# Optimization experiments

Measured on AMD Instinct MI355X. Metric: run time of the kernel, lower is better.

Reference implementation:

```python
import jax, jax.numpy as jnp
import numpy as np

B, S, D, H, HD = 2, 2048, 768, 12, 64


def setup_inputs() -> dict:
    key = jax.random.key(0)
    ks = jax.random.split(key, 8)
    w = lambda k, shp: jax.random.normal(k, shp, dtype=jnp.float32) * 0.02
    return {
        "hidden_states": jax.random.normal(ks[0], (B, S, D), dtype=jnp.float32),
        "Wq": w(ks[1], (D, D)), "bq": jnp.zeros((D,), jnp.float32),
        "Wk": w(ks[2], (D, D)), "bk": jnp.zeros((D,), jnp.float32),
        "Wv": w(ks[3], (D, D)), "bv": jnp.zeros((D,), jnp.float32),
        # hedgehog feature maps are initialized to identity in the module
        "Wfq": jnp.eye(HD, dtype=jnp.float32) + w(ks[4], (HD, HD)),
        "bfq": jnp.zeros((HD,), jnp.float32),
        "Wfk": jnp.eye(HD, dtype=jnp.float32) + w(ks[5], (HD, HD)),
        "bfk": jnp.zeros((HD,), jnp.float32),
    }


def _heads(x):
    # [B,S,D] -> [B,H,S,HD]
    return x.reshape(B, S, H, HD).transpose(0, 2, 1, 3)


def _feature_map(x, Wf, bf):
    # exp / exp(-x) hedgehog map: [B,H,S,HD] -> [B,H,S,2*HD]
    y = jnp.einsum('bhsd,ed->bhse', x, Wf) + bf
    return jnp.concatenate([jnp.exp(y), jnp.exp(-y)], axis=-1)


def reference(hidden_states, Wq, bq, Wk, bk, Wv, bv, Wfq, bfq, Wfk, bfk):
    h = hidden_states
    q = _heads(h @ Wq.T + bq)   # [B,H,S,HD]
    k = _heads(h @ Wk.T + bk)
    v = _heads(h @ Wv.T + bv)

    # frozen base (softmax) attention producing outputs + true_attns
    scale = 1.0 / np.sqrt(HD).astype(np.float32)
    scores = jnp.einsum('bhmd,bhnd->bhmn', q, k) * scale
    true_attns = jax.nn.softmax(scores, axis=-1)
    out = jnp.einsum('bhmn,bhnd->bhmd', true_attns, v)
    outputs = out.transpose(0, 2, 1, 3).reshape(B, S, D)

    # hedgehog predicted attention: quadratic linear attention
    fq = _feature_map(q, Wfq, bfq)  # [B,H,S,2*HD]
    fk = _feature_map(k, Wfk, bfk)
    qk = jnp.einsum('bhmd,bhnd->bhmn', fq, fk)
    pred_attns = qk / qk.sum(axis=-1, keepdims=True)

    return outputs, pred_attns, true_attns
```

## Files before the change

### kernel.cpp

```cpp
#include <hip/hip_runtime.h>
#include <math.h>

namespace {

constexpr int kB = 2, kS = 2048, kD = 768, kH = 12, kHD = 64, kF = 128, kBH = kB * kH;

typedef __attribute__((ext_vector_type(8))) short short8;
typedef __attribute__((ext_vector_type(4))) short short4v;
typedef __attribute__((ext_vector_type(4))) float f32x4;

__device__ __forceinline__ ushort f2bf(float x) {
    union { float f; unsigned u; } v; v.f = x;
    return (ushort)((v.u + 0x7fffu + ((v.u >> 16) & 1u)) >> 16);
}
__device__ __forceinline__ float bf2f(ushort u) {
    union { unsigned u; float f; } v; v.u = ((unsigned)u) << 16; return v.f;
}

__device__ __forceinline__ void gload16(const ushort* g, void* lds) {
    __builtin_amdgcn_global_load_lds(
        (const __attribute__((address_space(1))) void*)g,
        (__attribute__((address_space(3))) void*)lds, 16, 0, 0);
}

__device__ __forceinline__ void gstage64x64(ushort* ldsBase, const ushort* g,
                                            size_t strideElems, int w, int lane) {
    #pragma unroll
    for (int j = 0; j < 2; ++j) {
        const int row = 16 * w + 8 * j + (lane >> 3);
        const int chunk = lane & 7;
        const ushort* gp = g + (size_t)row * strideElems + ((chunk ^ (row & 7)) * 8);
        void* lp = (char*)ldsBase + (16 * w + 8 * j) * 128;
        gload16(gp, lp);
    }
}

__device__ __forceinline__ void gstageA128(ushort* ldsBase, const ushort* g,
                                           size_t strideElems, int w, int lane) {
    #pragma unroll
    for (int j = 0; j < 4; ++j) {
        const int row = 32 * w + 8 * j + (lane >> 3);
        const int chunk = lane & 7;
        const ushort* gp = g + (size_t)row * strideElems + ((chunk ^ (row & 7)) * 8);
        void* lp = (char*)ldsBase + (32 * w + 8 * j) * 128;
        gload16(gp, lp);
    }
}

__device__ __forceinline__ void gstage64x128(ushort* ldsBase, const ushort* g,
                                             int w, int lane) {
    #pragma unroll
    for (int j = 0; j < 4; ++j) {
        const int row = 16 * w + 4 * j + (lane >> 4);
        const int chunk = lane & 15;
        const ushort* gp = g + (size_t)row * kF + ((chunk ^ (row & 7)) * 8);
        void* lp = (char*)ldsBase + (16 * w + 4 * j) * 256;
        gload16(gp, lp);
    }
}

__device__ __forceinline__ void stage64x64(ushort* dst, const ushort* srcRow0,
                                           size_t rowStride, int t) {
    const int row = t >> 2, ce = (t & 3) * 16;
    const ushort* s = srcRow0 + (size_t)row * rowStride + ce;
    uint4 u0 = *(const uint4*)s;
    uint4 u1 = *(const uint4*)(s + 8);
    const int sw = (row & 7) << 4;
    *(uint4*)((char*)dst + row * 128 + ((ce * 2) ^ sw)) = u0;
    *(uint4*)((char*)dst + row * 128 + ((ce * 2 + 16) ^ sw)) = u1;
}

__device__ __forceinline__ void stage64x128(ushort* dst, const ushort* srcRow0, int t) {
    const int row = t >> 2, ce = (t & 3) * 32;
    const ushort* s = srcRow0 + (size_t)row * kF + ce;
    const int sw = (row & 7) << 4;
    #pragma unroll
    for (int u = 0; u < 4; ++u) {
        uint4 x = *(const uint4*)(s + u * 8);
        *(uint4*)((char*)dst + row * 256 + ((ce * 2 + u * 16) ^ sw)) = x;
    }
}

__global__ __launch_bounds__(256) void cast_kernel(
    const float* __restrict__ s0, const float* __restrict__ s1,
    const float* __restrict__ s2, const float* __restrict__ s3,
    ushort* __restrict__ d0, ushort* __restrict__ d1,
    ushort* __restrict__ d2, ushort* __restrict__ d3)
{
    const int seg = blockIdx.y;
    const float* src = seg == 0 ? s0 : seg == 1 ? s1 : seg == 2 ? s2 : s3;
    ushort* dst      = seg == 0 ? d0 : seg == 1 ? d1 : seg == 2 ? d2 : d3;
    const int n4 = (seg == 0 ? kB * kS * kD : kD * kD) / 4;
    for (int i = blockIdx.x * 256 + threadIdx.x; i < n4; i += gridDim.x * 256) {
        float4 v = *(const float4*)&src[(size_t)i * 4];
        short4v o;
        o[0] = (short)f2bf(v.x); o[1] = (short)f2bf(v.y);
        o[2] = (short)f2bf(v.z); o[3] = (short)f2bf(v.w);
        *(short4v*)&dst[(size_t)i * 4] = o;
    }
}

__global__ __launch_bounds__(256) void qkv_mfma_kernel(
    const ushort* __restrict__ hb,
    const ushort* __restrict__ Wqb, const ushort* __restrict__ Wkb,
    const ushort* __restrict__ Wvb,
    const float* __restrict__ bq, const float* __restrict__ bk,
    const float* __restrict__ bv,
    const float* __restrict__ Wfq, const float* __restrict__ bfq,
    const float* __restrict__ Wfk, const float* __restrict__ bfk,
    ushort* __restrict__ qd, ushort* __restrict__ kd, ushort* __restrict__ vTd,
    ushort* __restrict__ fqd, ushort* __restrict__ fkd,
    float* __restrict__ part)
{
    const int which = blockIdx.z;
    const ushort* __restrict__ Wb  = which == 0 ? Wqb : which == 1 ? Wkb : Wvb;
    const float* __restrict__ bias = which == 0 ? bq : which == 1 ? bk : bv;

    const int m0 = blockIdx.x * 128;
    const int n0 = blockIdx.y * 64;
    const int t = threadIdx.x, lane = t & 63, w = t >> 6;
    const int g = lane >> 4, ln = lane & 15;

    __shared__ __align__(16) ushort As[128 * 64];
    __shared__ __align__(16) ushort Bs[64 * 64];
    __shared__ __align__(16) ushort Ws[64 * 64];
    __shared__ float zsum[4][128];

    if (which < 2) {
        const float* __restrict__ Wf = (which == 0) ? Wfq : Wfk;
        const int row = t >> 2, ce = (t & 3) * 16;
        ushort tmp[16];
        #pragma unroll
        for (int c = 0; c < 16; c += 4) {
            float4 u = *(const float4*)&Wf[(size_t)row * 64 + ce + c];
            tmp[c + 0] = f2bf(u.x); tmp[c + 1] = f2bf(u.y);
            tmp[c + 2] = f2bf(u.z); tmp[c + 3] = f2bf(u.w);
        }
        const int sw = (row & 7) << 4;
        *(uint4*)((char*)Ws + row * 128 + ((ce * 2) ^ sw)) = *(uint4*)&tmp[0];
        *(uint4*)((char*)Ws + row * 128 + ((ce * 2 + 16) ^ sw)) = *(uint4*)&tmp[8];
    }

    f32x4 acc[2][4];
    #pragma unroll
    for (int rs = 0; rs < 2; ++rs)
        #pragma unroll
        for (int nt = 0; nt < 4; ++nt) acc[rs][nt] = (f32x4){0.f, 0.f, 0.f, 0.f};

    for (int k0 = 0; k0 < kD; k0 += 64) {
        gstageA128(As, hb + (size_t)m0 * kD + k0, kD, w, lane);
        gstage64x64(Bs, Wb + (size_t)n0 * kD + k0, kD, w, lane);
        asm volatile("s_waitcnt vmcnt(0)" ::: "memory");
        __builtin_amdgcn_sched_barrier(0);
        __builtin_amdgcn_s_barrier();

        short8 a[2][2], b[4][2];
        #pragma unroll
        for (int rs = 0; rs < 2; ++rs) {
            const int row = 32 * w + 16 * rs + ln, sw = (row & 7) << 4;
            #pragma unroll
            for (int kc = 0; kc < 2; ++kc)
                a[rs][kc] = *(const short8*)((const char*)As + row * 128 + ((kc * 64 + g * 16) ^ sw));
        }
        #pragma unroll
        for (int nt = 0; nt < 4; ++nt) {
            const int rk = nt * 16 + ln, sw = (rk & 7) << 4;
            #pragma unroll
            for (int kc = 0; kc < 2; ++kc)
                b[nt][kc] = *(const short8*)((const char*)Bs + rk * 128 + ((kc * 64 + g * 16) ^ sw));
        }
        #pragma unroll
        for (int rs = 0; rs < 2; ++rs)
            #pragma unroll
            for (int nt = 0; nt < 4; ++nt)
                #pragma unroll
                for (int kc = 0; kc < 2; ++kc)
                    acc[rs][nt] = __builtin_amdgcn_mfma_f32_16x16x32_bf16(
                        a[rs][kc], b[nt][kc], acc[rs][nt], 0, 0, 0);
        asm volatile("s_waitcnt lgkmcnt(0)" ::: "memory");
        __builtin_amdgcn_sched_barrier(0);
        __builtin_amdgcn_s_barrier();
    }

    const int hh = n0 >> 6;
    float bvn[4];
    #pragma unroll
    for (int nt = 0; nt < 4; ++nt) bvn[nt] = bias[n0 + nt * 16 + ln];

    if (which < 2) {
        ushort* __restrict__ dst = (which == 0) ? qd : kd;
        #pragma unroll
        for (int rs = 0; rs < 2; ++rs)
            #pragma unroll
            for (int nt = 0; nt < 4; ++nt)
                #pragma unroll
                for (int r = 0; r < 4; ++r) {
                    const int m = m0 + 32 * w + 16 * rs + g * 4 + r;
                    const int b_ = m >> 11, s_ = m & (kS - 1);
                    dst[((size_t)(b_ * kH + hh) * kS + s_) * kHD + nt * 16 + ln] =
                        f2bf(acc[rs][nt][r] + bvn[nt]);
                }
    } else {
        #pragma unroll
        for (int rs = 0; rs < 2; ++rs)
            #pragma unroll
            for (int nt = 0; nt < 4; ++nt) {
                const int m = m0 + 32 * w + 16 * rs + g * 4;
                const int b_ = m >> 11, s_ = m & (kS - 1);
                const int d = nt * 16 + ln;
                short4v o;
                #pragma unroll
                for (int r = 0; r < 4; ++r) o[r] = (short)f2bf(acc[rs][nt][r] + bvn[nt]);
                *(short4v*)&vTd[((size_t)(b_ * kH + hh) * kHD + d) * kS + s_] = o;
            }
    }

    if (which < 2) {
        __syncthreads();
        #pragma unroll
        for (int rs = 0; rs < 2; ++rs)
            #pragma unroll
            for (int nt = 0; nt < 4; ++nt)
                #pragma unroll
                for (int r = 0; r < 4; ++r) {
                    const int bm = 32 * w + 16 * rs + g * 4 + r;
                    const int e = nt * 16 + ln;
                    *(ushort*)((char*)As + bm * 128 + ((2 * e) ^ ((bm & 7) << 4))) =
                        f2bf(acc[rs][nt][r] + bvn[nt]);
                }
        __syncthreads();

        short8 a2[2][2], b2[4][2];
        #pragma unroll
        for (int rs = 0; rs < 2; ++rs) {
            const int row = 32 * w + 16 * rs + ln, sw = (row & 7) << 4;
            #pragma unroll
            for (int kc = 0; kc < 2; ++kc)
                a2[rs][kc] = *(const short8*)((const char*)As + row * 128 + ((kc * 64 + g * 16) ^ sw));
        }
        #pragma unroll
        for (int nt = 0; nt < 4; ++nt) {
            const int rk = nt * 16 + ln, sw = (rk & 7) << 4;
            #pragma unroll
            for (int kc = 0; kc < 2; ++kc)
                b2[nt][kc] = *(const short8*)((const char*)Ws + rk * 128 + ((kc * 64 + g * 16) ^ sw));
        }
        f32x4 yac[2][4];
        #pragma unroll
        for (int rs = 0; rs < 2; ++rs)
            #pragma unroll
            for (int nt = 0; nt < 4; ++nt) {
                yac[rs][nt] = (f32x4){0.f, 0.f, 0.f, 0.f};
                #pragma unroll
                for (int kc = 0; kc < 2; ++kc)
                    yac[rs][nt] = __builtin_amdgcn_mfma_f32_16x16x32_bf16(
                        a2[rs][kc], b2[nt][kc], yac[rs][nt], 0, 0, 0);
            }

        const float* __restrict__ bf2p = (which == 0) ? bfq : bfk;
        float bfv[4];
        #pragma unroll
        for (int nt = 0; nt < 4; ++nt) bfv[nt] = bf2p[nt * 16 + ln];

        ushort* __restrict__ dstF = (which == 0) ? fqd : fkd;
        float csp[4] = {0.f, 0.f, 0.f, 0.f}, csm[4] = {0.f, 0.f, 0.f, 0.f};
        #pragma unroll
        for (int rs = 0; rs < 2; ++rs)
            #pragma unroll
            for (int nt = 0; nt < 4; ++nt)
                #pragma unroll
                for (int r = 0; r < 4; ++r) {
                    const int m = m0 + 32 * w + 16 * rs + g * 4 + r;
                    const int b_ = m >> 11, s_ = m & (kS - 1);
                    const float y = yac[rs][nt][r] + bfv[nt];
                    const ushort hp = f2bf(__expf(y));
                    const ushort hm = f2bf(__expf(-y));
                    const size_t base =
                        ((size_t)(b_ * kH + hh) * kS + s_) * kF + nt * 16 + ln;
                    dstF[base] = hp;
                    dstF[base + 64] = hm;
                    if (which == 1) { csp[nt] += bf2f(hp); csm[nt] += bf2f(hm); }
                }

        if (which == 1) {
            #pragma unroll
            for (int nt = 0; nt < 4; ++nt) {
                csp[nt] += __shfl_xor(csp[nt], 16); csp[nt] += __shfl_xor(csp[nt], 32);
                csm[nt] += __shfl_xor(csm[nt], 16); csm[nt] += __shfl_xor(csm[nt], 32);
            }
            if (g == 0) {
                #pragma unroll
                for (int nt = 0; nt < 4; ++nt) {
                    zsum[w][nt * 16 + ln]      = csp[nt];
                    zsum[w][64 + nt * 16 + ln] = csm[nt];
                }
            }
            __syncthreads();
            if (t < 128) {
                const float s = zsum[0][t] + zsum[1][t] + zsum[2][t] + zsum[3][t];
                const int b_ = m0 >> 11, gr = (m0 & (kS - 1)) >> 7;
                part[((size_t)((b_ * kH + hh) * 16 + gr)) * kF + t] = s;
            }
        }
    }
}

__global__ __launch_bounds__(256) void true_attn_kernel(
    const ushort* __restrict__ q, const ushort* __restrict__ k,
    const ushort* __restrict__ vT,
    float* __restrict__ out0, float* __restrict__ out2)
{
    const int orig = blockIdx.y * 32 + blockIdx.x;
    const int swz  = (orig & 7) * 96 + (orig >> 3);
    const int bh = swz >> 5, m0 = (swz & 31) * 64;

    const int t = threadIdx.x, lane = t & 63, w = t >> 6;
    const int g = lane >> 4, ln = lane & 15;

    __shared__ __align__(16) ushort Qs[64 * 64];
    __shared__ __align__(16) ushort KVs[4 * 64 * 64];
    __shared__ __align__(16) ushort Ps[64 * 64];

    const ushort* __restrict__ qb = q  + (size_t)bh * kS * kHD;
    const ushort* __restrict__ kb = k  + (size_t)bh * kS * kHD;
    const ushort* __restrict__ vb = vT + (size_t)bh * kHD * kS;

    stage64x64(Qs, qb + (size_t)m0 * kHD, kHD, t);
    __syncthreads();

    short8 aq[2];
    {
        const int row = 16 * w + ln, sw = (row & 7) << 4;
        #pragma unroll
        for (int kc = 0; kc < 2; ++kc)
            aq[kc] = *(const short8*)((const char*)Qs + row * 128 + ((kc * 64 + g * 16) ^ sw));
    }

    gstage64x64(KVs, kb, kHD, w, lane);
    gstage64x64(KVs + 4096, kb + (size_t)64 * kHD, kHD, w, lane);
    float zacc[4] = {0.f, 0.f, 0.f, 0.f};
    for (int tt = 0; tt < 32; ++tt) {
        if (tt + 2 < 32) {
            gstage64x64(KVs + ((tt + 2) & 3) * 4096,
                        kb + (size_t)(tt + 2) * 64 * kHD, kHD, w, lane);
            asm volatile("s_waitcnt vmcnt(4)" ::: "memory");
        } else if (tt == 30) {
            asm volatile("s_waitcnt vmcnt(2)" ::: "memory");
        } else {
            asm volatile("s_waitcnt vmcnt(0)" ::: "memory");
        }
        __builtin_amdgcn_sched_barrier(0);
        __builtin_amdgcn_s_barrier();
        const ushort* KsC = KVs + (tt & 3) * 4096;
        #pragma unroll
        for (int nt = 0; nt < 4; ++nt) {
            f32x4 c = {0.f, 0.f, 0.f, 0.f};
            const int rk = nt * 16 + ln, sw = (rk & 7) << 4;
            #pragma unroll
            for (int kc = 0; kc < 2; ++kc) {
                short8 b = *(const short8*)((const char*)KsC + rk * 128 + ((kc * 64 + g * 16) ^ sw));
                c = __builtin_amdgcn_mfma_f32_16x16x32_bf16(aq[kc], b, c, 0, 0, 0);
            }
            #pragma unroll
            for (int r = 0; r < 4; ++r) zacc[r] += __expf(c[r] * 0.125f);
        }
    }
    float invl[4];
    #pragma unroll
    for (int r = 0; r < 4; ++r) {
        float z = zacc[r];
        z += __shfl_xor(z, 1); z += __shfl_xor(z, 2);
        z += __shfl_xor(z, 4); z += __shfl_xor(z, 8);
        invl[r] = 1.f / z;
    }
    __syncthreads();

    f32x4 accv[4];
    #pragma unroll
    for (int dt = 0; dt < 4; ++dt) accv[dt] = (f32x4){0.f, 0.f, 0.f, 0.f};

    gstage64x64(KVs, kb, kHD, w, lane);
    gstage64x64(KVs + 2 * 4096, vb, kS, w, lane);
    for (int tt = 0; tt < 32; ++tt) {
        const int cur = tt & 1;
        const int n0 = tt * 64;
        if (tt + 1 < 32) {
            gstage64x64(KVs + (cur ^ 1) * 4096,
                        kb + (size_t)(tt + 1) * 64 * kHD, kHD, w, lane);
            gstage64x64(KVs + (2 + (cur ^ 1)) * 4096,
                        vb + (tt + 1) * 64, kS, w, lane);
            asm volatile("s_waitcnt vmcnt(4)" ::: "memory");
        } else {
            asm volatile("s_waitcnt vmcnt(0)" ::: "memory");
        }
        __builtin_amdgcn_sched_barrier(0);
        __builtin_amdgcn_s_barrier();

        const ushort* KsC = KVs + cur * 4096;
        const ushort* VsC = KVs + (2 + cur) * 4096;
        #pragma unroll
        for (int nt = 0; nt < 4; ++nt) {
            f32x4 c = {0.f, 0.f, 0.f, 0.f};
            const int rk = nt * 16 + ln, sw = (rk & 7) << 4;
            #pragma unroll
            for (int kc = 0; kc < 2; ++kc) {
                short8 b = *(const short8*)((const char*)KsC + rk * 128 + ((kc * 64 + g * 16) ^ sw));
                c = __builtin_amdgcn_mfma_f32_16x16x32_bf16(aq[kc], b, c, 0, 0, 0);
            }
            #pragma unroll
            for (int r = 0; r < 4; ++r) {
                const int prow = 16 * w + g * 4 + r;
                const float p = __expf(c[r] * 0.125f) * invl[r];
                out2[((size_t)bh * kS + m0 + prow) * kS + n0 + nt * 16 + ln] = p;
                const int pb = prow * 128 + ((2 * (nt * 16 + ln)) ^ ((prow & 7) << 4));
                *(ushort*)((char*)Ps + pb) = f2bf(p);
            }
        }
        asm volatile("s_waitcnt lgkmcnt(0)" ::: "memory");
        __builtin_amdgcn_sched_barrier(0);

        const int rowp = 16 * w + ln, swp = (rowp & 7) << 4;
        #pragma unroll
        for (int kc = 0; kc < 2; ++kc) {
            short8 pa = *(const short8*)((const char*)Ps + rowp * 128 + ((kc * 64 + g * 16) ^ swp));
            #pragma unroll
            for (int dt = 0; dt < 4; ++dt) {
                const int rv = dt * 16 + ln, swv = (rv & 7) << 4;
                short8 bv = *(const short8*)((const char*)VsC + rv * 128 + ((kc * 64 + g * 16) ^ swv));
                accv[dt] = __builtin_amdgcn_mfma_f32_16x16x32_bf16(pa, bv, accv[dt], 0, 0, 0);
            }
        }
        __builtin_amdgcn_sched_barrier(0);
        __builtin_amdgcn_s_barrier();
    }

    const int b_ = bh / kH, h_ = bh % kH;
    #pragma unroll
    for (int dt = 0; dt < 4; ++dt)
        #pragma unroll
        for (int r = 0; r < 4; ++r) {
            const int prow = 16 * w + g * 4 + r;
            out0[((size_t)b_ * kS + m0 + prow) * kD + h_ * kHD + dt * 16 + ln] = accv[dt][r];
        }
}

__global__ __launch_bounds__(256) void pred_attn_kernel(
    const ushort* __restrict__ fq, const ushort* __restrict__ fk,
    const float* __restrict__ part, float* __restrict__ out1)
{
    const int orig = blockIdx.y * 32 + blockIdx.x;
    const int swz  = (orig & 7) * 96 + (orig >> 3);
    const int bh = swz >> 5, m0 = (swz & 31) * 64;

    const int t = threadIdx.x, lane = t & 63, w = t >> 6;
    const int g = lane >> 4, ln = lane & 15;

    __shared__ __align__(16) ushort Fq[64 * 128];
    __shared__ __align__(16) ushort Fk[2 * 64 * 128];
    __shared__ float fsum[128];
    __shared__ float invz[64];

    const ushort* __restrict__ fqb = fq + (size_t)bh * kS * kF;
    const ushort* __restrict__ fkb = fk + (size_t)bh * kS * kF;

    stage64x128(Fq, fqb + (size_t)m0 * kF, t);
    if (t < 128) {
        float s = 0.f;
        #pragma unroll
        for (int gg = 0; gg < 16; ++gg) s += part[((size_t)bh * 16 + gg) * kF + t];
        fsum[t] = s;
    }
    __syncthreads();

    short8 a[4];
    {
        const int row = 16 * w + ln, sw = (row & 7) << 4;
        #pragma unroll
        for (int kc = 0; kc < 4; ++kc)
            a[kc] = *(const short8*)((const char*)Fq + row * 256 + ((kc * 64 + g * 16) ^ sw));
    }

    float den = 0.f;
    #pragma unroll
    for (int kc = 0; kc < 4; ++kc)
        #pragma unroll
        for (int j = 0; j < 8; ++j)
            den += bf2f((ushort)a[kc][j]) * fsum[kc * 32 + g * 8 + j];
    den += __shfl_xor(den, 16);
    den += __shfl_xor(den, 32);
    if (g == 0) invz[16 * w + ln] = 1.f / den;
    __syncthreads();
    float invl[4];
    #pragma unroll
    for (int r = 0; r < 4; ++r) invl[r] = invz[16 * w + g * 4 + r];

    gstage64x128(Fk, fkb, w, lane);
    for (int tt = 0; tt < 32; ++tt) {
        const int cur = tt & 1;
        const int n0 = tt * 64;
        if (tt + 1 < 32) {
            gstage64x128(Fk + (cur ^ 1) * 8192, fkb + (size_t)(tt + 1) * 64 * kF, w, lane);
            asm volatile("s_waitcnt vmcnt(4)" ::: "memory");
        } else {
            asm volatile("s_waitcnt vmcnt(0)" ::: "memory");
        }
        __builtin_amdgcn_sched_barrier(0);
        __builtin_amdgcn_s_barrier();

        const ushort* FkC = Fk + cur * 8192;
        #pragma unroll
        for (int nt = 0; nt < 4; ++nt) {
            f32x4 c = {0.f, 0.f, 0.f, 0.f};
            const int rk = nt * 16 + ln, sw = (rk & 7) << 4;
            #pragma unroll
            for (int kc = 0; kc < 4; ++kc) {
                short8 b = *(const short8*)((const char*)FkC + rk * 256 + ((kc * 64 + g * 16) ^ sw));
                c = __builtin_amdgcn_mfma_f32_16x16x32_bf16(a[kc], b, c, 0, 0, 0);
            }
            #pragma unroll
            for (int r = 0; r < 4; ++r)
                out1[((size_t)bh * kS + m0 + 16 * w + g * 4 + r) * kS + n0 + nt * 16 + ln] =
                    c[r] * invl[r];
        }
        __builtin_amdgcn_sched_barrier(0);
        __builtin_amdgcn_s_barrier();
    }
}

}

extern "C" void kernel_launch(void* const* d_in, const int* in_sizes, int n_in,
                              void* d_out, int out_size, void* d_ws, size_t ws_size,
                              hipStream_t stream)
{
    (void)in_sizes; (void)n_in; (void)out_size; (void)ws_size;

    const float* hidden = (const float*)d_in[0];
    const float* Wq = (const float*)d_in[1];
    const float* bq = (const float*)d_in[2];
    const float* Wk = (const float*)d_in[3];
    const float* bk = (const float*)d_in[4];
    const float* Wv = (const float*)d_in[5];
    const float* bv = (const float*)d_in[6];
    const float* Wfq = (const float*)d_in[7];
    const float* bfq = (const float*)d_in[8];
    const float* Wfk = (const float*)d_in[9];
    const float* bfk = (const float*)d_in[10];

    float* out = (float*)d_out;
    float* out0 = out;
    float* out1 = out0 + (size_t)kB * kS * kD;
    float* out2 = out1 + (size_t)kBH * kS * kS;

    float* part = (float*)d_ws;
    ushort* hb  = (ushort*)(part + (size_t)kBH * 16 * kF);
    ushort* Wqb = hb  + (size_t)kB * kS * kD;
    ushort* Wkb = Wqb + (size_t)kD * kD;
    ushort* Wvb = Wkb + (size_t)kD * kD;
    ushort* qw  = Wvb + (size_t)kD * kD;
    ushort* kw  = qw  + (size_t)kBH * kS * kHD;
    ushort* vTw = kw  + (size_t)kBH * kS * kHD;
    ushort* fqw = vTw + (size_t)kBH * kS * kHD;
    ushort* fkw = fqw + (size_t)kBH * kS * kF;

    cast_kernel<<<dim3(512, 4), 256, 0, stream>>>(
        hidden, Wq, Wk, Wv, hb, Wqb, Wkb, Wvb);
    qkv_mfma_kernel<<<dim3(kB * kS / 128, kD / 64, 3), 256, 0, stream>>>(
        hb, Wqb, Wkb, Wvb, bq, bk, bv,
        Wfq, bfq, Wfk, bfk,
        qw, kw, vTw, fqw, fkw, part);
    true_attn_kernel<<<dim3(kS / 64, kBH), 256, 0, stream>>>(qw, kw, vTw, out0, out2);
    pred_attn_kernel<<<dim3(kS / 64, kBH), 256, 0, stream>>>(fqw, fkw, part, out1);
}
```

Measured before the change: 314.6 us.

## Split attention tiles across 8 waves with column-partitioned MFMA work

```diff
diff --git a/kernel.cpp b/kernel.cpp
--- a/kernel.cpp
+++ b/kernel.cpp
@@ -34,7 +34,6 @@
         gload16(gp, lp);
     }
 }
-
 __device__ __forceinline__ void gstageA128(ushort* ldsBase, const ushort* g,
                                            size_t strideElems, int w, int lane) {
     #pragma unroll
@@ -47,37 +46,21 @@
     }
 }
 
-__device__ __forceinline__ void gstage64x128(ushort* ldsBase, const ushort* g,
-                                             int w, int lane) {
-    #pragma unroll
-    for (int j = 0; j < 4; ++j) {
-        const int row = 16 * w + 4 * j + (lane >> 4);
+__device__ __forceinline__ void gstage8x64(ushort* ldsBase, const ushort* g,
+                                           size_t strideElems, int w, int lane) {
+    const int row = 8 * w + (lane >> 3);
+    const int chunk = lane & 7;
+    gload16(g + (size_t)row * strideElems + ((chunk ^ (row & 7)) * 8),
+            (char*)ldsBase + 8 * w * 128);
+}
+__device__ __forceinline__ void gstage8x128(ushort* ldsBase, const ushort* g,
+                                            int w, int lane) {
+    #pragma unroll
+    for (int j = 0; j < 2; ++j) {
+        const int row = 8 * w + 4 * j + (lane >> 4);
         const int chunk = lane & 15;
-        const ushort* gp = g + (size_t)row * kF + ((chunk ^ (row & 7)) * 8);
-        void* lp = (char*)ldsBase + (16 * w + 4 * j) * 256;
-        gload16(gp, lp);
-    }
-}
-
-__device__ __forceinline__ void stage64x64(ushort* dst, const ushort* srcRow0,
-                                           size_t rowStride, int t) {
-    const int row = t >> 2, ce = (t & 3) * 16;
-    const ushort* s = srcRow0 + (size_t)row * rowStride + ce;
-    uint4 u0 = *(const uint4*)s;
-    uint4 u1 = *(const uint4*)(s + 8);
-    const int sw = (row & 7) << 4;
-    *(uint4*)((char*)dst + row * 128 + ((ce * 2) ^ sw)) = u0;
-    *(uint4*)((char*)dst + row * 128 + ((ce * 2 + 16) ^ sw)) = u1;
-}
-
-__device__ __forceinline__ void stage64x128(ushort* dst, const ushort* srcRow0, int t) {
-    const int row = t >> 2, ce = (t & 3) * 32;
-    const ushort* s = srcRow0 + (size_t)row * kF + ce;
-    const int sw = (row & 7) << 4;
-    #pragma unroll
-    for (int u = 0; u < 4; ++u) {
-        uint4 x = *(const uint4*)(s + u * 8);
-        *(uint4*)((char*)dst + row * 256 + ((ce * 2 + u * 16) ^ sw)) = x;
+        gload16(g + (size_t)row * kF + ((chunk ^ (row & 7)) * 8),
+                (char*)ldsBase + (8 * w + 4 * j) * 256);
     }
 }
 
@@ -305,7 +288,7 @@
     }
 }
 
-__global__ __launch_bounds__(256) void true_attn_kernel(
+__global__ __launch_bounds__(512) void true_attn_kernel(
     const ushort* __restrict__ q, const ushort* __restrict__ k,
     const ushort* __restrict__ vT,
     float* __restrict__ out0, float* __restrict__ out2)
@@ -316,36 +299,42 @@
 
     const int t = threadIdx.x, lane = t & 63, w = t >> 6;
     const int g = lane >> 4, ln = lane & 15;
+    const int wr = w & 3, wc = w >> 2;
 
     __shared__ __align__(16) ushort Qs[64 * 64];
     __shared__ __align__(16) ushort KVs[4 * 64 * 64];
     __shared__ __align__(16) ushort Ps[64 * 64];
+    __shared__ float zl[8][16];
 
     const ushort* __restrict__ qb = q  + (size_t)bh * kS * kHD;
     const ushort* __restrict__ kb = k  + (size_t)bh * kS * kHD;
     const ushort* __restrict__ vb = vT + (size_t)bh * kHD * kS;
 
-    stage64x64(Qs, qb + (size_t)m0 * kHD, kHD, t);
+    {
+        const int row = t >> 3, ce = (t & 7) * 8;
+        uint4 u = *(const uint4*)(qb + (size_t)(m0 + row) * kHD + ce);
+        *(uint4*)((char*)Qs + row * 128 + ((ce * 2) ^ ((row & 7) << 4))) = u;
+    }
     __syncthreads();
 
     short8 aq[2];
     {
-        const int row = 16 * w + ln, sw = (row & 7) << 4;
+        const int row = 16 * wr + ln, sw = (row & 7) << 4;
         #pragma unroll
         for (int kc = 0; kc < 2; ++kc)
             aq[kc] = *(const short8*)((const char*)Qs + row * 128 + ((kc * 64 + g * 16) ^ sw));
     }
 
-    gstage64x64(KVs, kb, kHD, w, lane);
-    gstage64x64(KVs + 4096, kb + (size_t)64 * kHD, kHD, w, lane);
+    gstage8x64(KVs, kb, kHD, w, lane);
+    gstage8x64(KVs + 4096, kb + (size_t)64 * kHD, kHD, w, lane);
     float zacc[4] = {0.f, 0.f, 0.f, 0.f};
     for (int tt = 0; tt < 32; ++tt) {
         if (tt + 2 < 32) {
-            gstage64x64(KVs + ((tt + 2) & 3) * 4096,
-                        kb + (size_t)(tt + 2) * 64 * kHD, kHD, w, lane);
-            asm volatile("s_waitcnt vmcnt(4)" ::: "memory");
+            gstage8x64(KVs + ((tt + 2) & 3) * 4096,
+                       kb + (size_t)(tt + 2) * 64 * kHD, kHD, w, lane);
+            asm volatile("s_waitcnt vmcnt(2)" ::: "memory");
         } else if (tt == 30) {
-            asm volatile("s_waitcnt vmcnt(2)" ::: "memory");
+            asm volatile("s_waitcnt vmcnt(1)" ::: "memory");
         } else {
             asm volatile("s_waitcnt vmcnt(0)" ::: "memory");
         }
@@ -353,7 +342,8 @@
         __builtin_amdgcn_s_barrier();
         const ushort* KsC = KVs + (tt & 3) * 4096;
         #pragma unroll
-        for (int nt = 0; nt < 4; ++nt) {
+        for (int h2 = 0; h2 < 2; ++h2) {
+            const int nt = 2 * wc + h2;
             f32x4 c = {0.f, 0.f, 0.f, 0.f};
             const int rk = nt * 16 + ln, sw = (rk & 7) << 4;
             #pragma unroll
@@ -365,31 +355,38 @@
             for (int r = 0; r < 4; ++r) zacc[r] += __expf(c[r] * 0.125f);
         }
     }
-    float invl[4];
     #pragma unroll
     for (int r = 0; r < 4; ++r) {
         float z = zacc[r];
         z += __shfl_xor(z, 1); z += __shfl_xor(z, 2);
         z += __shfl_xor(z, 4); z += __shfl_xor(z, 8);
-        invl[r] = 1.f / z;
+        zacc[r] = z;
+    }
+    if (ln == 0) {
+        #pragma unroll
+        for (int r = 0; r < 4; ++r) zl[w][g * 4 + r] = zacc[r];
     }
     __syncthreads();
-
-    f32x4 accv[4];
-    #pragma unroll
-    for (int dt = 0; dt < 4; ++dt) accv[dt] = (f32x4){0.f, 0.f, 0.f, 0.f};
-
-    gstage64x64(KVs, kb, kHD, w, lane);
-    gstage64x64(KVs + 2 * 4096, vb, kS, w, lane);
+    float invl[4];
+    #pragma unroll
+    for (int r = 0; r < 4; ++r)
+        invl[r] = 1.f / (zl[wr][g * 4 + r] + zl[4 + wr][g * 4 + r]);
+
+    f32x4 accv[2];
+    accv[0] = (f32x4){0.f, 0.f, 0.f, 0.f};
+    accv[1] = (f32x4){0.f, 0.f, 0.f, 0.f};
+
+    gstage8x64(KVs, kb, kHD, w, lane);
+    gstage8x64(KVs + 2 * 4096, vb, kS, w, lane);
     for (int tt = 0; tt < 32; ++tt) {
         const int cur = tt & 1;
         const int n0 = tt * 64;
         if (tt + 1 < 32) {
-            gstage64x64(KVs + (cur ^ 1) * 4096,
-                        kb + (size_t)(tt + 1) * 64 * kHD, kHD, w, lane);
-            gstage64x64(KVs + (2 + (cur ^ 1)) * 4096,
-                        vb + (tt + 1) * 64, kS, w, lane);
-            asm volatile("s_waitcnt vmcnt(4)" ::: "memory");
+            gstage8x64(KVs + (cur ^ 1) * 4096,
+                       kb + (size_t)(tt + 1) * 64 * kHD, kHD, w, lane);
+            gstage8x64(KVs + (2 + (cur ^ 1)) * 4096,
+                       vb + (tt + 1) * 64, kS, w, lane);
+            asm volatile("s_waitcnt vmcnt(2)" ::: "memory");
         } else {
             asm volatile("s_waitcnt vmcnt(0)" ::: "memory");
         }
@@ -399,7 +396,8 @@
         const ushort* KsC = KVs + cur * 4096;
         const ushort* VsC = KVs + (2 + cur) * 4096;
         #pragma unroll
-        for (int nt = 0; nt < 4; ++nt) {
+        for (int h2 = 0; h2 < 2; ++h2) {
+            const int nt = 2 * wc + h2;
             f32x4 c = {0.f, 0.f, 0.f, 0.f};
             const int rk = nt * 16 + ln, sw = (rk & 7) << 4;
             #pragma unroll
@@ -409,7 +407,7 @@
             }
             #pragma unroll
             for (int r = 0; r < 4; ++r) {
-                const int prow = 16 * w + g * 4 + r;
+                const int prow = 16 * wr + g * 4 + r;
                 const float p = __expf(c[r] * 0.125f) * invl[r];
                 out2[((size_t)bh * kS + m0 + prow) * kS + n0 + nt * 16 + ln] = p;
                 const int pb = prow * 128 + ((2 * (nt * 16 + ln)) ^ ((prow & 7) << 4));
@@ -418,16 +416,18 @@
         }
         asm volatile("s_waitcnt lgkmcnt(0)" ::: "memory");
         __builtin_amdgcn_sched_barrier(0);
-
-        const int rowp = 16 * w + ln, swp = (rowp & 7) << 4;
+        __builtin_amdgcn_s_barrier();
+
+        const int rowp = 16 * wr + ln, swp = (rowp & 7) << 4;
         #pragma unroll
         for (int kc = 0; kc < 2; ++kc) {
             short8 pa = *(const short8*)((const char*)Ps + rowp * 128 + ((kc * 64 + g * 16) ^ swp));
             #pragma unroll
-            for (int dt = 0; dt < 4; ++dt) {
+            for (int d2 = 0; d2 < 2; ++d2) {
+                const int dt = 2 * wc + d2;
                 const int rv = dt * 16 + ln, swv = (rv & 7) << 4;
                 short8 bv = *(const short8*)((const char*)VsC + rv * 128 + ((kc * 64 + g * 16) ^ swv));
-                accv[dt] = __builtin_amdgcn_mfma_f32_16x16x32_bf16(pa, bv, accv[dt], 0, 0, 0);
+                accv[d2] = __builtin_amdgcn_mfma_f32_16x16x32_bf16(pa, bv, accv[d2], 0, 0, 0);
             }
         }
         __builtin_amdgcn_sched_barrier(0);
@@ -436,15 +436,16 @@
 
     const int b_ = bh / kH, h_ = bh % kH;
     #pragma unroll
-    for (int dt = 0; dt < 4; ++dt)
+    for (int d2 = 0; d2 < 2; ++d2)
         #pragma unroll
         for (int r = 0; r < 4; ++r) {
-            const int prow = 16 * w + g * 4 + r;
-            out0[((size_t)b_ * kS + m0 + prow) * kD + h_ * kHD + dt * 16 + ln] = accv[dt][r];
-        }
-}
-
-__global__ __launch_bounds__(256) void pred_attn_kernel(
+            const int prow = 16 * wr + g * 4 + r;
+            const int dt = 2 * wc + d2;
+            out0[((size_t)b_ * kS + m0 + prow) * kD + h_ * kHD + dt * 16 + ln] = accv[d2][r];
+        }
+}
+
+__global__ __launch_bounds__(512) void pred_attn_kernel(
     const ushort* __restrict__ fq, const ushort* __restrict__ fk,
     const float* __restrict__ part, float* __restrict__ out1)
 {
@@ -454,6 +455,7 @@
 
     const int t = threadIdx.x, lane = t & 63, w = t >> 6;
     const int g = lane >> 4, ln = lane & 15;
+    const int wr = w & 3, wc = w >> 2;
 
     __shared__ __align__(16) ushort Fq[64 * 128];
     __shared__ __align__(16) ushort Fk[2 * 64 * 128];
@@ -463,7 +465,13 @@
     const ushort* __restrict__ fqb = fq + (size_t)bh * kS * kF;
     const ushort* __restrict__ fkb = fk + (size_t)bh * kS * kF;
 
-    stage64x128(Fq, fqb + (size_t)m0 * kF, t);
+    {
+        const int row = t >> 3, ce = (t & 7) * 16;
+        const ushort* s = fqb + (size_t)(m0 + row) * kF + ce;
+        const int sw = (row & 7) << 4;
+        *(uint4*)((char*)Fq + row * 256 + ((ce * 2) ^ sw)) = *(const uint4*)s;
+        *(uint4*)((char*)Fq + row * 256 + ((ce * 2 + 16) ^ sw)) = *(const uint4*)(s + 8);
+    }
     if (t < 128) {
         float s = 0.f;
         #pragma unroll
@@ -474,7 +482,7 @@
 
     short8 a[4];
     {
-        const int row = 16 * w + ln, sw = (row & 7) << 4;
+        const int row = 16 * wr + ln, sw = (row & 7) << 4;
         #pragma unroll
         for (int kc = 0; kc < 4; ++kc)
             a[kc] = *(const short8*)((const char*)Fq + row * 256 + ((kc * 64 + g * 16) ^ sw));
@@ -488,19 +496,19 @@
             den += bf2f((ushort)a[kc][j]) * fsum[kc * 32 + g * 8 + j];
     den += __shfl_xor(den, 16);
     den += __shfl_xor(den, 32);
-    if (g == 0) invz[16 * w + ln] = 1.f / den;
+    if (g == 0) invz[16 * wr + ln] = 1.f / den;
     __syncthreads();
     float invl[4];
     #pragma unroll
-    for (int r = 0; r < 4; ++r) invl[r] = invz[16 * w + g * 4 + r];
-
-    gstage64x128(Fk, fkb, w, lane);
+    for (int r = 0; r < 4; ++r) invl[r] = invz[16 * wr + g * 4 + r];
+
+    gstage8x128(Fk, fkb, w, lane);
     for (int tt = 0; tt < 32; ++tt) {
         const int cur = tt & 1;
         const int n0 = tt * 64;
         if (tt + 1 < 32) {
-            gstage64x128(Fk + (cur ^ 1) * 8192, fkb + (size_t)(tt + 1) * 64 * kF, w, lane);
-            asm volatile("s_waitcnt vmcnt(4)" ::: "memory");
+            gstage8x128(Fk + (cur ^ 1) * 8192, fkb + (size_t)(tt + 1) * 64 * kF, w, lane);
+            asm volatile("s_waitcnt vmcnt(2)" ::: "memory");
         } else {
             asm volatile("s_waitcnt vmcnt(0)" ::: "memory");
         }
@@ -509,7 +517,8 @@
 
         const ushort* FkC = Fk + cur * 8192;
         #pragma unroll
-        for (int nt = 0; nt < 4; ++nt) {
+        for (int h2 = 0; h2 < 2; ++h2) {
+            const int nt = 2 * wc + h2;
             f32x4 c = {0.f, 0.f, 0.f, 0.f};
             const int rk = nt * 16 + ln, sw = (rk & 7) << 4;
             #pragma unroll
@@ -519,7 +528,7 @@
             }
             #pragma unroll
             for (int r = 0; r < 4; ++r)
-                out1[((size_t)bh * kS + m0 + 16 * w + g * 4 + r) * kS + n0 + nt * 16 + ln] =
+                out1[((size_t)bh * kS + m0 + 16 * wr + g * 4 + r) * kS + n0 + nt * 16 + ln] =
                     c[r] * invl[r];
         }
         __builtin_amdgcn_sched_barrier(0);
@@ -569,6 +578,6 @@
         hb, Wqb, Wkb, Wvb, bq, bk, bv,
         Wfq, bfq, Wfk, bfk,
         qw, kw, vTw, fqw, fkw, part);
-    true_attn_kernel<<<dim3(kS / 64, kBH), 256, 0, stream>>>(qw, kw, vTw, out0, out2);
-    pred_attn_kernel<<<dim3(kS / 64, kBH), 256, 0, stream>>>(fqw, fkw, part, out1);
-}
+    true_attn_kernel<<<dim3(kS / 64, kBH), 512, 0, stream>>>(qw, kw, vTw, out0, out2);
+    pred_attn_kernel<<<dim3(kS / 64, kBH), 512, 0, stream>>>(fqw, fkw, part, out1);
+}
```

Measured after the change: 301.0 us. -4.3%, faster.
